# Kernel optimization log

Hardware: AMD Instinct MI355X
Metric: run time of the kernel (lower is better)

The kernel has to match this reference:

```python
import math
import jax, jax.numpy as jnp
import numpy as np

B, S, HID = 2, 1024, 4096
NH, NKV, HD = 32, 8, 128
G = NH // NKV            # query heads per KV head (GQA group size)
PAST = 1024              # tokens already in the cache per sequence
L = PAST + S             # total KV tokens attended per sequence
SLOTS = 16384            # paged KV-cache slots (flat token addressing)
MAXPOS = 8192
THETA = 10000.0


def _rope_table():
    inv_freq = 1.0 / (THETA ** (np.arange(0, HD, 2, dtype=np.float64) / HD))
    freqs = np.arange(MAXPOS, dtype=np.float64)[:, None] * inv_freq[None, :]
    emb = np.concatenate([freqs, freqs], axis=-1)          # [MAXPOS, HD]
    return jnp.asarray(np.stack([np.cos(emb), np.sin(emb)], axis=1), jnp.float32)  # [MAXPOS,2,HD]


def setup_inputs() -> dict:
    key = jax.random.key(0)
    ks = jax.random.split(key, 6)
    hidden_states = jax.random.normal(ks[0], (B, S, HID), jnp.float32)
    kv_cache = jax.random.normal(ks[1], (SLOTS, 2, NKV, HD), jnp.float32)  # [slot, k/v, kv_head, hd]
    rope_cache = _rope_table()
    Wq = jax.random.normal(ks[2], (HID, NH * HD), jnp.float32) * 0.02
    Wk = jax.random.normal(ks[3], (HID, NKV * HD), jnp.float32) * 0.02
    Wv = jax.random.normal(ks[4], (HID, NKV * HD), jnp.float32) * 0.02
    Wo = jax.random.normal(ks[5], (NH * HD, HID), jnp.float32) * 0.02
    position_offsets = jnp.full((B,), PAST, jnp.int32)
    base = jnp.arange(B, dtype=jnp.int32)[:, None] * L            # each seq owns L contiguous slots
    kv_drain_addr_lut = base + PAST + jnp.arange(S, dtype=jnp.int32)[None, :]  # [B,S] write addrs
    kv_lut = base + jnp.arange(L, dtype=jnp.int32)[None, :]                    # [B,L] read addrs
    return {
        "hidden_states": hidden_states, "kv_cache": kv_cache, "rope_cache": rope_cache,
        "Wq": Wq, "Wk": Wk, "Wv": Wv, "Wo": Wo,
        "position_offsets": position_offsets,
        "kv_drain_addr_lut": kv_drain_addr_lut, "kv_lut": kv_lut,
    }


def _apply_rope(x, cos, sin):
    # x: [B, H, S, HD]; cos/sin: [B, 1, S, HD]
    x1, x2 = x[..., : HD // 2], x[..., HD // 2:]
    return x * cos + jnp.concatenate([-x2, x1], axis=-1) * sin


def reference(hidden_states, kv_cache, rope_cache, Wq, Wk, Wv, Wo,
              position_offsets, kv_drain_addr_lut, kv_lut):
    # QKV projections
    q = (hidden_states @ Wq).reshape(B, S, NH, HD).transpose(0, 2, 1, 3)    # [B,NH,S,HD]
    k = (hidden_states @ Wk).reshape(B, S, NKV, HD).transpose(0, 2, 1, 3)   # [B,NKV,S,HD]
    v = (hidden_states @ Wv).reshape(B, S, NKV, HD).transpose(0, 2, 1, 3)
    # RoPE at absolute positions
    pos = position_offsets[:, None] + jnp.arange(S, dtype=jnp.int32)        # [B,S]
    cos = rope_cache[pos, 0][:, None]                                       # [B,1,S,HD]
    sin = rope_cache[pos, 1][:, None]
    q = _apply_rope(q, cos, sin)
    k = _apply_rope(k, cos, sin)
    # LUT-addressed KV-cache drain (copy_kv_block)
    k_tok = k.transpose(0, 2, 1, 3).reshape(B * S, NKV, HD)
    v_tok = v.transpose(0, 2, 1, 3).reshape(B * S, NKV, HD)
    lut = kv_drain_addr_lut.reshape(-1)
    kv_cache = kv_cache.at[lut, 0].set(k_tok).at[lut, 1].set(v_tok)
    # Gather per-sequence KV pages and run grouped (GQA) causal attention
    kv = kv_cache[kv_lut]                                                   # [B,L,2,NKV,HD]
    keys = kv[:, :, 0].transpose(0, 2, 1, 3)                                # [B,NKV,L,HD]
    vals = kv[:, :, 1].transpose(0, 2, 1, 3)
    qg = q.reshape(B, NKV, G, S, HD)
    scores = jnp.einsum('bhgsd,bhld->bhgsl', qg, keys) * (HD ** -0.5)       # [B,NKV,G,S,L]
    kpos = jnp.arange(L, dtype=jnp.int32)
    causal = kpos[None, None, :] <= pos[:, :, None]                         # [B,S,L]
    scores = jnp.where(causal[:, None, None], scores, jnp.float32(-1e30))
    p = jax.nn.softmax(scores, axis=-1)
    out = jnp.einsum('bhgsl,bhld->bhgsd', p, vals).reshape(B, NH, S, HD)
    out = out.transpose(0, 2, 1, 3).reshape(B, S, HID)
    return out @ Wo
```

## Files before the change

kernel.cpp:

```cpp
#include <hip/hip_runtime.h>
#include <hip/hip_bf16.h>
#include <cstdint>
#include <cstddef>

#define B_    2
#define S_    1024
#define HID_  4096
#define NH_   32
#define NKV_  8
#define HD_   128
#define G_    4
#define PAST_ 1024
#define L_    2048
#define NQKV_ 6144

typedef __bf16 bf16_t;
typedef bf16_t bf16x4 __attribute__((ext_vector_type(4)));
typedef bf16_t bf16x8 __attribute__((ext_vector_type(8)));
typedef float  f32x4  __attribute__((ext_vector_type(4)));
typedef unsigned short ushort4_t __attribute__((ext_vector_type(4)));

__device__ __forceinline__ void gload_lds16(const bf16_t* g, bf16_t* l) {
  __builtin_amdgcn_global_load_lds(
      (const __attribute__((address_space(1))) void*)g,
      (__attribute__((address_space(3))) void*)l, 16, 0, 0);
}

__global__ __launch_bounds__(256) void cvt_bf16x8(const float* __restrict__ src,
                                                  bf16_t* __restrict__ dst) {
  size_t i = ((size_t)blockIdx.x * 256 + threadIdx.x) * 8;
  f32x4 a = *(const f32x4*)(src + i);
  f32x4 b = *(const f32x4*)(src + i + 4);
  bf16x8 o;
#pragma unroll
  for (int j = 0; j < 4; ++j) o[j] = (bf16_t)a[j];
#pragma unroll
  for (int j = 0; j < 4; ++j) o[4 + j] = (bf16_t)b[j];
  *(bf16x8*)(dst + i) = o;
}

__global__ __launch_bounds__(256) void wt_all(const float* __restrict__ Wq,
                                              const float* __restrict__ Wk,
                                              const float* __restrict__ Wv,
                                              const float* __restrict__ Wo,
                                              bf16_t* __restrict__ Wcat,
                                              bf16_t* __restrict__ Wot) {
  __shared__ float T[64][65];
  const int tid = threadIdx.x;
  const int bx = blockIdx.x;
  const float* src;
  bf16_t* dst;
  int C, c0;
  if (bx < 64)      { src = Wq; dst = Wcat;                         C = 4096; c0 = bx * 64; }
  else if (bx < 80) { src = Wk; dst = Wcat + (size_t)4096 * 4096;   C = 1024; c0 = (bx - 64) * 64; }
  else if (bx < 96) { src = Wv; dst = Wcat + (size_t)5120 * 4096;   C = 1024; c0 = (bx - 80) * 64; }
  else              { src = Wo; dst = Wot;                          C = 4096; c0 = (bx - 96) * 64; }
  const int r0 = blockIdx.y * 64;
  const int rr = tid >> 4;
  const int c4 = tid & 15;
#pragma unroll
  for (int i = 0; i < 4; ++i) {
    int row = i * 16 + rr;
    f32x4 v = *(const f32x4*)&src[(size_t)(r0 + row) * C + c0 + c4 * 4];
#pragma unroll
    for (int e = 0; e < 4; ++e) T[row][c4 * 4 + e] = v[e];
  }
  __syncthreads();
#pragma unroll
  for (int i = 0; i < 4; ++i) {
    int orow = i * 16 + rr;
    ushort4_t o;
#pragma unroll
    for (int e = 0; e < 4; ++e) {
      union { bf16_t b; unsigned short u; } cv;
      cv.b = (bf16_t)T[c4 * 4 + e][orow];
      o[e] = cv.u;
    }
    *(ushort4_t*)&dst[(size_t)(c0 + orow) * 4096 + r0 + c4 * 4] = o;
  }
}

template <int BN, bool OUT_BF16>
__global__ __launch_bounds__(512) void gemm8(const bf16_t* __restrict__ A,
                                             const bf16_t* __restrict__ Bt,
                                             void* __restrict__ C, int N, int K) {
  constexpr int BSLAB = BN * 32;
  constexpr int BUFE = 16384 + 2 * BSLAB;
  constexpr int NF = BN / 64;
  constexpr int WN = BN / 4;
  constexpr int BCH = BN * 4;
  __shared__ bf16_t sm[2 * BUFE];

  const int tid = threadIdx.x;
  const int lane = tid & 63;
  const int w = tid >> 6;
  const int wm = w >> 2, wn = w & 3;
  const int g = lane >> 4;
  const int r16 = lane & 15;

  const int flat = blockIdx.y * 32 + blockIdx.x;
  const int xcd = flat & 7;
  const int i2 = flat >> 3;
  const int tx = xcd * 4 + (i2 & 3);
  const int ty = i2 >> 2;
  const int m0 = ty * 256;
  const int n0 = tx * BN;

  const int NT = K >> 6;

  f32x4 acc[8][NF] = {};

  auto stageA = [&](int T, int j) {
    bf16_t* base = sm + (T & 1) * BUFE + j * 8192;
#pragma unroll
    for (int cj = 0; cj < 2; ++cj) {
      int c = (w * 2 + cj) * 64 + lane;
      int p = c * 16;
      int l = p ^ (((p >> 9) & 1) << 5);
      int row = l >> 6, colb = l & 63;
      gload_lds16(A + (size_t)(m0 + row) * K + T * 64 + j * 32 + (colb >> 1),
                  base + (w * 2 + cj) * 512);
    }
  };
  auto stageB = [&](int T, int j) {
    bf16_t* base = sm + (T & 1) * BUFE + 16384 + j * BSLAB;
#pragma unroll
    for (int cj = 0; cj < (BCH + 511) / 512; ++cj) {
      int cbase = cj * 512 + w * 64;
      if (cbase < BCH) {
        int c = cbase + lane;
        int p = c * 16;
        int l = p ^ (((p >> 9) & 1) << 5);
        int row = l >> 6, colb = l & 63;
        gload_lds16(Bt + (size_t)(n0 + row) * K + T * 64 + j * 32 + (colb >> 1),
                    base + cbase * 8);
      }
    }
  };
  auto waitbar = [&]() {
    if (BN == 192) {
      if (w < 4) asm volatile("s_waitcnt vmcnt(4)" ::: "memory");
      else       asm volatile("s_waitcnt vmcnt(3)" ::: "memory");
    } else {
      asm volatile("s_waitcnt vmcnt(3)" ::: "memory");
    }
    asm volatile("s_barrier" ::: "memory");
  };

  stageA(0, 0); stageB(0, 0);
  stageA(0, 1); stageB(0, 1);
  waitbar();

#pragma unroll 2
  for (int T = 0; T < NT; ++T) {
    const bf16_t* abuf = sm + (T & 1) * BUFE;
    const bf16_t* bbuf = abuf + 16384;
#pragma unroll
    for (int j = 0; j < 2; ++j) {
      const bf16_t* as = abuf + j * 8192;
      const bf16_t* bs = bbuf + j * BSLAB;
      bf16x8 af[8];
      bf16x8 bfr[NF];
#pragma unroll
      for (int m = 0; m < 8; ++m) {
        int a = (wm * 128 + m * 16 + r16) * 64 + g * 16;
        a ^= ((a >> 9) & 1) << 5;
        af[m] = *(const bf16x8*)((const char*)as + a);
      }
#pragma unroll
      for (int n = 0; n < NF; ++n) {
        int a = (wn * WN + n * 16 + r16) * 64 + g * 16;
        a ^= ((a >> 9) & 1) << 5;
        bfr[n] = *(const bf16x8*)((const char*)bs + a);
      }
      if (T + 1 < NT) { stageA(T + 1, j); stageB(T + 1, j); }
      __builtin_amdgcn_s_setprio(1);
#pragma unroll
      for (int m = 0; m < 8; ++m)
#pragma unroll
        for (int n = 0; n < NF; ++n)
          acc[m][n] = __builtin_amdgcn_mfma_f32_16x16x32_bf16(af[m], bfr[n],
                                                              acc[m][n], 0, 0, 0);
      __builtin_amdgcn_s_setprio(0);
      waitbar();
    }
  }

#pragma unroll
  for (int m = 0; m < 8; ++m)
#pragma unroll
    for (int n = 0; n < NF; ++n)
#pragma unroll
      for (int r = 0; r < 4; ++r) {
        int row = m0 + wm * 128 + m * 16 + g * 4 + r;
        int col = n0 + wn * WN + n * 16 + r16;
        if (OUT_BF16)
          ((bf16_t*)C)[(size_t)row * N + col] = (bf16_t)acc[m][n][r];
        else
          ((float*)C)[(size_t)row * N + col] = acc[m][n][r];
      }
}

__global__ __launch_bounds__(256) void rope_pack(const bf16_t* __restrict__ QKV,
                                                 const float* __restrict__ rope,
                                                 bf16_t* __restrict__ Qb,
                                                 bf16_t* __restrict__ Kb) {
  const int tok = blockIdx.x;
  const int head = blockIdx.y * 2 + (threadIdx.x >> 7);
  const int d = threadIdx.x & 127;
  const int b = tok >> 10, s = tok & 1023;
  const int pos = PAST_ + s;
  const int off = head < NH_ ? head * HD_ : HID_ + (head - NH_) * HD_;
  const bf16_t* row = QKV + (size_t)tok * NQKV_;
  float x = (float)row[off + d];
  int dp = d < 64 ? d + 64 : d - 64;
  float xp = (float)row[off + dp];
  float c = rope[(size_t)(pos * 2) * HD_ + d];
  float sn = rope[(size_t)(pos * 2 + 1) * HD_ + d];
  float out = d < 64 ? x * c - xp * sn : x * c + xp * sn;
  if (head < NH_)
    Qb[((size_t)(b * NH_ + head) * S_ + s) * HD_ + d] = (bf16_t)out;
  else
    Kb[((size_t)(b * NKV_ + (head - NH_)) * L_ + PAST_ + s) * HD_ + d] = (bf16_t)out;
}

__global__ __launch_bounds__(256) void past_kv(const float* __restrict__ cache,
                                               const int* __restrict__ kv_lut,
                                               bf16_t* __restrict__ Kb,
                                               bf16_t* __restrict__ Vt) {
  __shared__ bf16_t Vs[128][72];
  const int tid = threadIdx.x;
  const int lt = blockIdx.x & 15;
  const int h = (blockIdx.x >> 4) & 7;
  const int b = blockIdx.x >> 7;
  const int l0 = lt * 64;
#pragma unroll
  for (int i = 0; i < 32; ++i) {
    int idx = i * 256 + tid;
    int l = idx >> 7, d = idx & 127;
    int slot = kv_lut[b * L_ + l0 + l];
    float kv = cache[((size_t)slot * 2 * NKV_ + h) * HD_ + d];
    float vv = cache[(((size_t)slot * 2 + 1) * NKV_ + h) * HD_ + d];
    Kb[((size_t)(b * NKV_ + h) * L_ + l0 + l) * HD_ + d] = (bf16_t)kv;
    Vs[d][l] = (bf16_t)vv;
  }
  __syncthreads();
#pragma unroll
  for (int i = 0; i < 32; ++i) {
    int idx = i * 256 + tid;
    int d = idx >> 6, l = idx & 63;
    Vt[((size_t)(b * NKV_ + h) * HD_ + d) * L_ + l0 + l] = Vs[d][l];
  }
}

__global__ __launch_bounds__(256) void v_pack(const bf16_t* __restrict__ QKV,
                                              bf16_t* __restrict__ Vt) {
  __shared__ bf16_t Vs[128][72];
  const int tid = threadIdx.x;
  const int st = blockIdx.x & 15;
  const int h = (blockIdx.x >> 4) & 7;
  const int b = blockIdx.x >> 7;
  const int s0 = st * 64;
#pragma unroll
  for (int i = 0; i < 32; ++i) {
    int idx = i * 256 + tid;
    int sl = idx >> 7, d = idx & 127;
    Vs[d][sl] = QKV[(size_t)(b * S_ + s0 + sl) * NQKV_ + HID_ + NKV_ * HD_ + h * HD_ + d];
  }
  __syncthreads();
#pragma unroll
  for (int i = 0; i < 32; ++i) {
    int idx = i * 256 + tid;
    int d = idx >> 6, l = idx & 63;
    Vt[((size_t)(b * NKV_ + h) * HD_ + d) * L_ + PAST_ + s0 + l] = Vs[d][l];
  }
}

__global__ __launch_bounds__(512, 4) void attn(const bf16_t* __restrict__ Qb,
                                               const bf16_t* __restrict__ Kb,
                                               const bf16_t* __restrict__ Vt,
                                               bf16_t* __restrict__ Ctx) {
  __shared__ bf16_t smem[32768];

  const int tid = threadIdx.x;
  const int lane = tid & 63;
  const int w = tid >> 6;
  const int g = lane >> 4;
  const int r16 = lane & 15;
  const int rx = r16 & 7;

  const int id = blockIdx.x;
  const int kh = id & 7;
  const int b = (id >> 3) & 1;
  const int qh = (id >> 4) & 3;
  const int grp = id >> 6;
  const int qc = grp < 4 ? 7 - grp : grp - 4;
  const int h = kh * G_ + qh;

  const int s0w = qc * 128 + w * 16;

  const bf16_t* qp = Qb + ((size_t)(b * NH_ + h) * S_ + s0w + r16) * HD_ + g * 8;
  bf16x8 qf[4];
#pragma unroll
  for (int ks = 0; ks < 4; ++ks) qf[ks] = *(const bf16x8*)(qp + ks * 32);

  const bf16_t* kbase = Kb + (size_t)(b * NKV_ + kh) * L_ * HD_;
  const bf16_t* vbase = Vt + (size_t)(b * NKV_ + kh) * HD_ * L_;

  const int slot0 = w * 2;
  const int kl0 = slot0 * 4 + (lane >> 4);
  const int kc0 = (lane & 15) ^ (kl0 & 7);
  const int kl1 = kl0 + 4;
  const int kc1 = (lane & 15) ^ (kl1 & 7);
  const int vd0 = slot0 * 8 + (lane >> 3);
  const int vc0 = (lane & 7) ^ (vd0 & 7);
  const int vd1 = vd0 + 8;
  const int vc1 = (lane & 7) ^ (vd1 & 7);

  float m_run = -1e30f;
  float s_run = 0.f;
  f32x4 acc_o[8] = {};

  const float scale = 0.08838834764831845f;
  const int qpos_base = PAST_ + s0w;
  const int qpos = qpos_base + r16;
  const int nt_ = 18 + 2 * qc;

  {
    bf16_t* Kd = smem;
    bf16_t* Vd = smem + 16384;
    gload_lds16(kbase + (size_t)kl0 * HD_ + kc0 * 8, Kd + slot0 * 512);
    gload_lds16(kbase + (size_t)kl1 * HD_ + kc1 * 8, Kd + (slot0 + 1) * 512);
    gload_lds16(vbase + (size_t)vd0 * L_ + vc0 * 8, Vd + slot0 * 512);
    gload_lds16(vbase + (size_t)vd1 * L_ + vc1 * 8, Vd + (slot0 + 1) * 512);
  }
  __syncthreads();

  for (int t = 0; t < nt_; ++t) {
    const int cur = t & 1;
    const int lt = t * 64;

    if (t + 1 < nt_) {
      const int ltn = lt + 64;
      bf16_t* Kd = smem + (cur ^ 1) * 8192;
      bf16_t* Vd = smem + 16384 + (cur ^ 1) * 8192;
      gload_lds16(kbase + (size_t)(ltn + kl0) * HD_ + kc0 * 8, Kd + slot0 * 512);
      gload_lds16(kbase + (size_t)(ltn + kl1) * HD_ + kc1 * 8, Kd + (slot0 + 1) * 512);
      gload_lds16(vbase + (size_t)vd0 * L_ + ltn + vc0 * 8, Vd + slot0 * 512);
      gload_lds16(vbase + (size_t)vd1 * L_ + ltn + vc1 * 8, Vd + (slot0 + 1) * 512);
    }

    const bf16_t* Kc = smem + cur * 8192;
    const bf16_t* Vc = smem + 16384 + cur * 8192;

    f32x4 sc[4] = {};
#pragma unroll
    for (int nt = 0; nt < 4; ++nt) {
#pragma unroll
      for (int ks = 0; ks < 4; ++ks) {
        bf16x8 kf = *(const bf16x8*)&Kc[(nt * 16 + r16) * 128 + (((ks * 4 + g) ^ rx) << 3)];
        sc[nt] = __builtin_amdgcn_mfma_f32_16x16x32_bf16(kf, qf[ks], sc[nt], 0, 0, 0);
      }
    }

    const bool need_mask = (lt + 63) > qpos_base;
    float sv[4][4];
    float tmax = -1e30f;
#pragma unroll
    for (int nt = 0; nt < 4; ++nt)
#pragma unroll
      for (int r = 0; r < 4; ++r) {
        float v = sc[nt][r] * scale;
        if (need_mask) {
          int l = lt + nt * 16 + g * 4 + r;
          if (l > qpos) v = -1e30f;
        }
        sv[nt][r] = v;
        tmax = fmaxf(tmax, v);
      }
    tmax = fmaxf(tmax, __shfl_xor(tmax, 16, 64));
    tmax = fmaxf(tmax, __shfl_xor(tmax, 32, 64));

    if (!__all(tmax <= m_run + 8.f)) {
      float newm = fmaxf(m_run, tmax);
      float alpha = __expf(m_run - newm);
      m_run = newm;
      s_run *= alpha;
#pragma unroll
      for (int r = 0; r < 4; ++r) {
        float a = __shfl(alpha, g * 4 + r, 64);
#pragma unroll
        for (int d8 = 0; d8 < 8; ++d8) acc_o[d8][r] *= a;
      }
    }

    uint32_t pkw[4][2];
    float psum = 0.f;
#pragma unroll
    for (int nt = 0; nt < 4; ++nt) {
      union { bf16_t bh[4]; uint32_t u[2]; } pk;
#pragma unroll
      for (int r = 0; r < 4; ++r) {
        float pv = __expf(sv[nt][r] - m_run);
        psum += pv;
        pk.bh[r] = (bf16_t)pv;
      }
      pkw[nt][0] = pk.u[0];
      pkw[nt][1] = pk.u[1];
    }
    psum += __shfl_xor(psum, 16, 64);
    psum += __shfl_xor(psum, 32, 64);
    s_run += psum;

    const bool hi = (g & 2) != 0;
    const int srcA = ((g & 1) << 5) + r16;
#pragma unroll
    for (int ks2 = 0; ks2 < 2; ++ks2) {
      uint32_t a00 = (uint32_t)__shfl((int)pkw[2 * ks2][0],     srcA,      64);
      uint32_t a01 = (uint32_t)__shfl((int)pkw[2 * ks2][1],     srcA,      64);
      uint32_t b00 = (uint32_t)__shfl((int)pkw[2 * ks2 + 1][0], srcA,      64);
      uint32_t b01 = (uint32_t)__shfl((int)pkw[2 * ks2 + 1][1], srcA,      64);
      uint32_t a10 = (uint32_t)__shfl((int)pkw[2 * ks2][0],     srcA + 16, 64);
      uint32_t a11 = (uint32_t)__shfl((int)pkw[2 * ks2][1],     srcA + 16, 64);
      uint32_t b10 = (uint32_t)__shfl((int)pkw[2 * ks2 + 1][0], srcA + 16, 64);
      uint32_t b11 = (uint32_t)__shfl((int)pkw[2 * ks2 + 1][1], srcA + 16, 64);
      union { uint32_t u[4]; bf16x8 v; } pa;
      pa.u[0] = hi ? b00 : a00;
      pa.u[1] = hi ? b01 : a01;
      pa.u[2] = hi ? b10 : a10;
      pa.u[3] = hi ? b11 : a11;
#pragma unroll
      for (int d8 = 0; d8 < 8; ++d8) {
        bf16x8 vf = *(const bf16x8*)&Vc[(d8 * 16 + r16) * 64 + (((ks2 * 4 + g) ^ rx) << 3)];
        acc_o[d8] = __builtin_amdgcn_mfma_f32_16x16x32_bf16(pa.v, vf, acc_o[d8], 0, 0, 0);
      }
    }

    __syncthreads();
  }

  float inv[4];
#pragma unroll
  for (int r = 0; r < 4; ++r) inv[r] = 1.f / __shfl(s_run, g * 4 + r, 64);
#pragma unroll
  for (int d8 = 0; d8 < 8; ++d8)
#pragma unroll
    for (int r = 0; r < 4; ++r) {
      int tok = b * S_ + s0w + g * 4 + r;
      int col = h * HD_ + d8 * 16 + r16;
      Ctx[(size_t)tok * HID_ + col] = (bf16_t)(acc_o[d8][r] * inv[r]);
    }
}

extern "C" void kernel_launch(void* const* d_in, const int* in_sizes, int n_in,
                              void* d_out, int out_size, void* d_ws, size_t ws_size,
                              hipStream_t stream) {
  const float* hidden = (const float*)d_in[0];
  const float* kv_cache = (const float*)d_in[1];
  const float* rope = (const float*)d_in[2];
  const float* Wq = (const float*)d_in[3];
  const float* Wk = (const float*)d_in[4];
  const float* Wv = (const float*)d_in[5];
  const float* Wo = (const float*)d_in[6];
  const int* kv_lut = (const int*)d_in[9];
  float* out = (float*)d_out;

  bf16_t* Xb = (bf16_t*)d_ws;
  bf16_t* Wcat = Xb + (size_t)2048 * 4096;
  bf16_t* Wot = Wcat + (size_t)6144 * 4096;
  bf16_t* QKVb = Wot + (size_t)4096 * 4096;
  bf16_t* Qb = QKVb + (size_t)2048 * 6144;
  bf16_t* Kb = Qb + (size_t)B_ * NH_ * S_ * HD_;
  bf16_t* Vt = Kb + (size_t)B_ * NKV_ * L_ * HD_;
  bf16_t* Ctx = Xb;

  cvt_bf16x8<<<4096, 256, 0, stream>>>(hidden, Xb);
  wt_all<<<dim3(160, 64), 256, 0, stream>>>(Wq, Wk, Wv, Wo, Wcat, Wot);

  gemm8<192, true><<<dim3(32, 8), 512, 0, stream>>>(Xb, Wcat, QKVb, NQKV_, HID_);

  rope_pack<<<dim3(2048, 20), 256, 0, stream>>>(QKVb, rope, Qb, Kb);
  past_kv<<<256, 256, 0, stream>>>(kv_cache, kv_lut, Kb, Vt);
  v_pack<<<256, 256, 0, stream>>>(QKVb, Vt);

  attn<<<512, 512, 0, stream>>>(Qb, Kb, Vt, Ctx);

  gemm8<128, false><<<dim3(32, 8), 512, 0, stream>>>(Ctx, Wot, out, HID_, HID_);
}
```

Baseline: 354.7 us.

## Feed fp32 Wo directly into output GEMM and route attention P through LDS

Result: no change. 355.9 us (+0.4%).

```diff
diff --git a/kernel.cpp b/kernel.cpp
--- a/kernel.cpp
+++ b/kernel.cpp
@@ -42,9 +42,7 @@
 __global__ __launch_bounds__(256) void wt_all(const float* __restrict__ Wq,
                                               const float* __restrict__ Wk,
                                               const float* __restrict__ Wv,
-                                              const float* __restrict__ Wo,
-                                              bf16_t* __restrict__ Wcat,
-                                              bf16_t* __restrict__ Wot) {
+                                              bf16_t* __restrict__ Wcat) {
   __shared__ float T[64][65];
   const int tid = threadIdx.x;
   const int bx = blockIdx.x;
@@ -53,8 +51,7 @@
   int C, c0;
   if (bx < 64)      { src = Wq; dst = Wcat;                         C = 4096; c0 = bx * 64; }
   else if (bx < 80) { src = Wk; dst = Wcat + (size_t)4096 * 4096;   C = 1024; c0 = (bx - 64) * 64; }
-  else if (bx < 96) { src = Wv; dst = Wcat + (size_t)5120 * 4096;   C = 1024; c0 = (bx - 80) * 64; }
-  else              { src = Wo; dst = Wot;                          C = 4096; c0 = (bx - 96) * 64; }
+  else              { src = Wv; dst = Wcat + (size_t)5120 * 4096;   C = 1024; c0 = (bx - 80) * 64; }
   const int r0 = blockIdx.y * 64;
   const int rr = tid >> 4;
   const int c4 = tid & 15;
@@ -198,6 +195,111 @@
           ((bf16_t*)C)[(size_t)row * N + col] = (bf16_t)acc[m][n][r];
         else
           ((float*)C)[(size_t)row * N + col] = acc[m][n][r];
+      }
+}
+
+__global__ __launch_bounds__(512) void gemm8f(const bf16_t* __restrict__ A,
+                                              const float* __restrict__ Bw,
+                                              float* __restrict__ C, int N, int K) {
+  __shared__ bf16_t smA[32768];
+  __shared__ float  smB[16384];
+
+  const int tid = threadIdx.x;
+  const int lane = tid & 63;
+  const int w = tid >> 6;
+  const int wm = w >> 2, wn = w & 3;
+  const int g = lane >> 4;
+  const int r16 = lane & 15;
+
+  const int flat = blockIdx.y * 32 + blockIdx.x;
+  const int xcd = flat & 7;
+  const int i2 = flat >> 3;
+  const int tx = xcd * 4 + (i2 & 3);
+  const int ty = i2 >> 2;
+  const int m0 = ty * 256;
+  const int n0 = tx * 128;
+
+  const int NT = K >> 6;
+
+  f32x4 acc[8][2] = {};
+
+  auto stageA = [&](int T, int j) {
+    bf16_t* base = smA + (T & 1) * 16384 + j * 8192;
+#pragma unroll
+    for (int cj = 0; cj < 2; ++cj) {
+      int c = (w * 2 + cj) * 64 + lane;
+      int p = c * 16;
+      int l = p ^ (((p >> 9) & 1) << 5);
+      int row = l >> 6, colb = l & 63;
+      gload_lds16(A + (size_t)(m0 + row) * K + T * 64 + j * 32 + (colb >> 1),
+                  base + (w * 2 + cj) * 512);
+    }
+  };
+  auto stageB = [&](int T, int j) {
+    float* base = smB + (T & 1) * 8192 + j * 4096;
+#pragma unroll
+    for (int cj = 0; cj < 2; ++cj) {
+      int c = (w * 2 + cj) * 64 + lane;
+      int row = c >> 5;
+      int c16 = (c & 31) ^ ((row >> 3) << 2);
+      gload_lds16((const bf16_t*)(Bw + (size_t)(T * 64 + j * 32 + row) * N +
+                                  n0 + c16 * 4),
+                  (bf16_t*)(base + (w * 2 + cj) * 256));
+    }
+  };
+  auto waitbar = [&]() {
+    asm volatile("s_waitcnt vmcnt(4)" ::: "memory");
+    asm volatile("s_barrier" ::: "memory");
+  };
+
+  stageA(0, 0); stageB(0, 0);
+  stageA(0, 1); stageB(0, 1);
+  waitbar();
+
+#pragma unroll 2
+  for (int T = 0; T < NT; ++T) {
+#pragma unroll
+    for (int j = 0; j < 2; ++j) {
+      const bf16_t* as = smA + (T & 1) * 16384 + j * 8192;
+      const float* bs = smB + (T & 1) * 8192 + j * 4096;
+      bf16x8 af[8];
+      bf16x8 bfr[2];
+#pragma unroll
+      for (int m = 0; m < 8; ++m) {
+        int a = (wm * 128 + m * 16 + r16) * 64 + g * 16;
+        a ^= ((a >> 9) & 1) << 5;
+        af[m] = *(const bf16x8*)((const char*)as + a);
+      }
+#pragma unroll
+      for (int n = 0; n < 2; ++n) {
+        int col = wn * 32 + n * 16 + r16;
+        int cidx = ((((col >> 2) ^ (g << 2)) << 2) | (col & 3));
+#pragma unroll
+        for (int i = 0; i < 8; ++i)
+          bfr[n][i] = (bf16_t)bs[(g * 8 + i) * 128 + cidx];
+      }
+      if (T + 1 < NT) { stageA(T + 1, j); stageB(T + 1, j); }
+      __builtin_amdgcn_s_setprio(1);
+#pragma unroll
+      for (int m = 0; m < 8; ++m)
+#pragma unroll
+        for (int n = 0; n < 2; ++n)
+          acc[m][n] = __builtin_amdgcn_mfma_f32_16x16x32_bf16(af[m], bfr[n],
+                                                              acc[m][n], 0, 0, 0);
+      __builtin_amdgcn_s_setprio(0);
+      waitbar();
+    }
+  }
+
+#pragma unroll
+  for (int m = 0; m < 8; ++m)
+#pragma unroll
+    for (int n = 0; n < 2; ++n)
+#pragma unroll
+      for (int r = 0; r < 4; ++r) {
+        int row = m0 + wm * 128 + m * 16 + g * 4 + r;
+        int col = n0 + wn * 32 + n * 16 + r16;
+        C[(size_t)row * N + col] = acc[m][n][r];
       }
 }
 
@@ -276,11 +378,11 @@
   }
 }
 
-__global__ __launch_bounds__(512, 4) void attn(const bf16_t* __restrict__ Qb,
-                                               const bf16_t* __restrict__ Kb,
-                                               const bf16_t* __restrict__ Vt,
-                                               bf16_t* __restrict__ Ctx) {
-  __shared__ bf16_t smem[32768];
+__global__ __launch_bounds__(512) void attn(const bf16_t* __restrict__ Qb,
+                                            const bf16_t* __restrict__ Kb,
+                                            const bf16_t* __restrict__ Vt,
+                                            bf16_t* __restrict__ Ctx) {
+  __shared__ bf16_t smem[40960];
 
   const int tid = threadIdx.x;
   const int lane = tid & 63;
@@ -352,6 +454,7 @@
 
     const bf16_t* Kc = smem + cur * 8192;
     const bf16_t* Vc = smem + 16384 + cur * 8192;
+    bf16_t* Pw = smem + 32768 + w * 1024;
 
     f32x4 sc[4] = {};
 #pragma unroll
@@ -394,45 +497,29 @@
       }
     }
 
-    uint32_t pkw[4][2];
     float psum = 0.f;
 #pragma unroll
     for (int nt = 0; nt < 4; ++nt) {
-      union { bf16_t bh[4]; uint32_t u[2]; } pk;
+      bf16x4 pk;
 #pragma unroll
       for (int r = 0; r < 4; ++r) {
         float pv = __expf(sv[nt][r] - m_run);
         psum += pv;
-        pk.bh[r] = (bf16_t)pv;
-      }
-      pkw[nt][0] = pk.u[0];
-      pkw[nt][1] = pk.u[1];
+        pk[r] = (bf16_t)pv;
+      }
+      *(bf16x4*)&Pw[r16 * 64 + (((nt * 2 + (g >> 1)) ^ rx) << 3) + (g & 1) * 4] = pk;
     }
     psum += __shfl_xor(psum, 16, 64);
     psum += __shfl_xor(psum, 32, 64);
     s_run += psum;
 
-    const bool hi = (g & 2) != 0;
-    const int srcA = ((g & 1) << 5) + r16;
 #pragma unroll
     for (int ks2 = 0; ks2 < 2; ++ks2) {
-      uint32_t a00 = (uint32_t)__shfl((int)pkw[2 * ks2][0],     srcA,      64);
-      uint32_t a01 = (uint32_t)__shfl((int)pkw[2 * ks2][1],     srcA,      64);
-      uint32_t b00 = (uint32_t)__shfl((int)pkw[2 * ks2 + 1][0], srcA,      64);
-      uint32_t b01 = (uint32_t)__shfl((int)pkw[2 * ks2 + 1][1], srcA,      64);
-      uint32_t a10 = (uint32_t)__shfl((int)pkw[2 * ks2][0],     srcA + 16, 64);
-      uint32_t a11 = (uint32_t)__shfl((int)pkw[2 * ks2][1],     srcA + 16, 64);
-      uint32_t b10 = (uint32_t)__shfl((int)pkw[2 * ks2 + 1][0], srcA + 16, 64);
-      uint32_t b11 = (uint32_t)__shfl((int)pkw[2 * ks2 + 1][1], srcA + 16, 64);
-      union { uint32_t u[4]; bf16x8 v; } pa;
-      pa.u[0] = hi ? b00 : a00;
-      pa.u[1] = hi ? b01 : a01;
-      pa.u[2] = hi ? b10 : a10;
-      pa.u[3] = hi ? b11 : a11;
+      bf16x8 pa = *(const bf16x8*)&Pw[r16 * 64 + (((ks2 * 4 + g) ^ rx) << 3)];
 #pragma unroll
       for (int d8 = 0; d8 < 8; ++d8) {
         bf16x8 vf = *(const bf16x8*)&Vc[(d8 * 16 + r16) * 64 + (((ks2 * 4 + g) ^ rx) << 3)];
-        acc_o[d8] = __builtin_amdgcn_mfma_f32_16x16x32_bf16(pa.v, vf, acc_o[d8], 0, 0, 0);
+        acc_o[d8] = __builtin_amdgcn_mfma_f32_16x16x32_bf16(pa, vf, acc_o[d8], 0, 0, 0);
       }
     }
 
@@ -467,15 +554,14 @@
 
   bf16_t* Xb = (bf16_t*)d_ws;
   bf16_t* Wcat = Xb + (size_t)2048 * 4096;
-  bf16_t* Wot = Wcat + (size_t)6144 * 4096;
-  bf16_t* QKVb = Wot + (size_t)4096 * 4096;
+  bf16_t* QKVb = Wcat + (size_t)6144 * 4096;
   bf16_t* Qb = QKVb + (size_t)2048 * 6144;
   bf16_t* Kb = Qb + (size_t)B_ * NH_ * S_ * HD_;
   bf16_t* Vt = Kb + (size_t)B_ * NKV_ * L_ * HD_;
   bf16_t* Ctx = Xb;
 
   cvt_bf16x8<<<4096, 256, 0, stream>>>(hidden, Xb);
-  wt_all<<<dim3(160, 64), 256, 0, stream>>>(Wq, Wk, Wv, Wo, Wcat, Wot);
+  wt_all<<<dim3(96, 64), 256, 0, stream>>>(Wq, Wk, Wv, Wcat);
 
   gemm8<192, true><<<dim3(32, 8), 512, 0, stream>>>(Xb, Wcat, QKVb, NQKV_, HID_);
 
@@ -485,5 +571,5 @@
 
   attn<<<512, 512, 0, stream>>>(Qb, Kb, Vt, Ctx);
 
-  gemm8<128, false><<<dim3(32, 8), 512, 0, stream>>>(Ctx, Wot, out, HID_, HID_);
-}
+  gemm8f<<<dim3(32, 8), 512, 0, stream>>>(Ctx, Wo, out, HID_, HID_);
+}
```
